# Optimization experiments

Hardware: AMD Instinct MI355X
Metric: run time of the kernel (lower is better)

Reference implementation:

```python
import jax, jax.numpy as jnp
import numpy as np

DIM = 512; HEADS = 8; DH = 64; M = 256; ITERS = 6; N_PATCH = 10000; N_CLASSES = 2


def layernorm(x, w, b, eps=1e-5):
    mu = x.mean(-1, keepdims=True)
    var = ((x - mu) ** 2).mean(-1, keepdims=True)
    return (x - mu) * jax.lax.rsqrt(var + eps) * w + b


def pinv_iter(x, iters=ITERS):
    # Moore-Penrose iterative pseudo-inverse (lucidrains nystrom-attention)
    abs_x = jnp.abs(x)
    col = abs_x.sum(-1)
    row = abs_x.sum(-2)
    z = jnp.swapaxes(x, -1, -2) / (jnp.max(col) * jnp.max(row))
    I = jnp.eye(x.shape[-1], dtype=x.dtype)
    for _ in range(iters):
        xz = x @ z
        z = 0.25 * z @ (13 * I - xz @ (15 * I - xz @ (7 * I - xz)))
    return z


def nystrom_attn(x, qkv_w, out_w, out_b, res_w):
    b, n, _ = x.shape
    pad = (-n) % M  # front-pad so n divisible by num_landmarks
    xp = jnp.pad(x, ((0, 0), (pad, 0), (0, 0)))
    npad = n + pad
    qkv = (xp @ qkv_w).reshape(b, npad, 3, HEADS, DH)
    q = jnp.transpose(qkv[:, :, 0], (0, 2, 1, 3)) * (DH ** -0.5)  # [b,h,n,d]
    k = jnp.transpose(qkv[:, :, 1], (0, 2, 1, 3))
    v = jnp.transpose(qkv[:, :, 2], (0, 2, 1, 3))
    l = npad // M
    q_l = q.reshape(b, HEADS, M, l, DH).mean(3)  # landmark means [b,h,m,d]
    k_l = k.reshape(b, HEADS, M, l, DH).mean(3)
    attn1 = jax.nn.softmax(jnp.einsum('bhnd,bhmd->bhnm', q, k_l), -1)
    attn2 = jax.nn.softmax(jnp.einsum('bhid,bhjd->bhij', q_l, k_l), -1)
    attn3 = jax.nn.softmax(jnp.einsum('bhmd,bhnd->bhmn', q_l, k), -1)
    out = (attn1 @ pinv_iter(attn2)) @ (attn3 @ v)  # [b,h,n,d]
    pk = (res_w.shape[2] - 1) // 2
    out = out + jax.lax.conv_general_dilated(
        v, res_w, (1, 1), [(pk, pk), (0, 0)], feature_group_count=HEADS)
    out = jnp.transpose(out, (0, 2, 1, 3)).reshape(b, npad, HEADS * DH)
    out = out @ out_w + out_b
    return out[:, -n:]


def ppeg(x, H, W, w7, b7, w5, b5, w3, b3):
    B, _, C = x.shape
    cls_tok, feat = x[:, :1], x[:, 1:]
    f = jnp.transpose(feat, (0, 2, 1)).reshape(B, C, H, W)
    def dw(w, b):
        p = w.shape[2] // 2
        return jax.lax.conv_general_dilated(
            f, w, (1, 1), [(p, p), (p, p)], feature_group_count=C) + b[None, :, None, None]
    y = f + dw(w7, b7) + dw(w5, b5) + dw(w3, b3)
    y = jnp.transpose(y.reshape(B, C, H * W), (0, 2, 1))
    return jnp.concatenate([cls_tok, y], axis=1)


def setup_inputs() -> dict:
    key = jax.random.key(0)
    ks = jax.random.split(key, 16)
    d = {
        'x': jax.random.normal(ks[0], (1, N_PATCH, DIM), jnp.float32),
        'cls_token': jax.random.normal(ks[1], (1, 1, DIM), jnp.float32) * 1e-6,
        'ln1_w': jnp.ones((DIM,), jnp.float32), 'ln1_b': jnp.zeros((DIM,), jnp.float32),
        'qkv1_w': jax.random.normal(ks[2], (DIM, 3 * DIM), jnp.float32) * 0.03,
        'out1_w': jax.random.normal(ks[3], (DIM, DIM), jnp.float32) * 0.04,
        'out1_b': jnp.zeros((DIM,), jnp.float32),
        'res1_w': jax.random.normal(ks[4], (HEADS, 1, 33, 1), jnp.float32) * 0.1,
        'p7_w': jax.random.normal(ks[5], (DIM, 1, 7, 7), jnp.float32) * 0.1,
        'p7_b': jnp.zeros((DIM,), jnp.float32),
        'p5_w': jax.random.normal(ks[6], (DIM, 1, 5, 5), jnp.float32) * 0.1,
        'p5_b': jnp.zeros((DIM,), jnp.float32),
        'p3_w': jax.random.normal(ks[7], (DIM, 1, 3, 3), jnp.float32) * 0.1,
        'p3_b': jnp.zeros((DIM,), jnp.float32),
        'ln2_w': jnp.ones((DIM,), jnp.float32), 'ln2_b': jnp.zeros((DIM,), jnp.float32),
        'qkv2_w': jax.random.normal(ks[8], (DIM, 3 * DIM), jnp.float32) * 0.03,
        'out2_w': jax.random.normal(ks[9], (DIM, DIM), jnp.float32) * 0.04,
        'out2_b': jnp.zeros((DIM,), jnp.float32),
        'res2_w': jax.random.normal(ks[10], (HEADS, 1, 33, 1), jnp.float32) * 0.1,
        'norm_w': jnp.ones((DIM,), jnp.float32), 'norm_b': jnp.zeros((DIM,), jnp.float32),
        'fc2_w': jax.random.normal(ks[11], (DIM, N_CLASSES), jnp.float32) * 0.06,
        'fc2_b': jnp.zeros((N_CLASSES,), jnp.float32),
        'pc_w': jax.random.normal(ks[12], (DIM, N_CLASSES), jnp.float32) * 0.06,
        'pc_b': jnp.zeros((N_CLASSES,), jnp.float32),
    }
    return d


def reference(x, cls_token, ln1_w, ln1_b, qkv1_w, out1_w, out1_b, res1_w,
              p7_w, p7_b, p5_w, p5_b, p3_w, p3_b,
              ln2_w, ln2_b, qkv2_w, out2_w, out2_b, res2_w,
              norm_w, norm_b, fc2_w, fc2_b, pc_w, pc_b):
    h = x.astype(jnp.float32)
    B, n0, C = h.shape
    _H = int(np.ceil(np.sqrt(n0))); _W = _H
    add = _H * _W - n0
    if add > 0:
        h = jnp.concatenate([h, h[:, :add]], axis=1)
    h = jnp.concatenate([jnp.broadcast_to(cls_token, (B, 1, C)), h], axis=1)
    h = h + nystrom_attn(layernorm(h, ln1_w, ln1_b), qkv1_w, out1_w, out1_b, res1_w)
    h = ppeg(h, _H, _W, p7_w, p7_b, p5_w, p5_b, p3_w, p3_b)
    h = h + nystrom_attn(layernorm(h, ln2_w, ln2_b), qkv2_w, out2_w, out2_b, res2_w)
    hn = layernorm(h, norm_w, norm_b)
    cls_f = hn[:, 0]
    patch_f = hn[:, 1:]
    if add > 0:
        patch_f = patch_f[:, :n0]
    bag_logits = cls_f @ fc2_w + fc2_b
    patch_logits = patch_f @ pc_w + pc_b
    patch_scores = jax.nn.softmax(patch_logits, -1)
    return bag_logits, patch_logits, patch_scores
```

## Files before the change

kernel.cpp:

```cpp
#include <hip/hip_runtime.h>
#include <hip/hip_bf16.h>

#define DIM    512
#define HEADS  8
#define DHD    64
#define MLAND  256
#define NTOK   10001
#define NPATCH 10000
#define NPAD   10240
#define PADR   239
#define LFAC   40
#define MOUT   10112
#define NSPLIT 8

typedef __bf16 bf16x8_t __attribute__((ext_vector_type(8)));
typedef float  f32x4_t  __attribute__((ext_vector_type(4)));
typedef short  short8_t __attribute__((ext_vector_type(8)));

__device__ inline bf16x8_t bzero8() {
    union { short8_t s; bf16x8_t b; } u;
    u.s = (short8_t){0, 0, 0, 0, 0, 0, 0, 0};
    return u.b;
}

#define GLDS(gp, lp) __builtin_amdgcn_global_load_lds( \
    (const __attribute__((address_space(1))) void*)(gp), \
    (__attribute__((address_space(3))) void*)(lp), 16, 0, 0)

__global__ void k_concat(const float* __restrict__ x, const float* __restrict__ cls,
                         float* __restrict__ h) {
    int idx = blockIdx.x * 256 + threadIdx.x;
    if (idx >= NTOK * DIM) return;
    int row = idx / DIM, col = idx % DIM;
    h[idx] = (row == 0) ? cls[col] : x[(row - 1) * DIM + col];
}

__global__ void k_layernorm_bf(const float* __restrict__ h, const float* __restrict__ w,
                               const float* __restrict__ b, __hip_bfloat16* __restrict__ xbf) {
    int row = blockIdx.x;
    const float* r = h + (long)row * DIM;
    int t = threadIdx.x;
    float v0 = r[t], v1 = r[t + 256];
    __shared__ float red[256];
    red[t] = v0 + v1; __syncthreads();
    for (int o = 128; o > 0; o >>= 1) { if (t < o) red[t] += red[t + o]; __syncthreads(); }
    float mu = red[0] * (1.f / DIM); __syncthreads();
    float d0 = v0 - mu, d1 = v1 - mu;
    red[t] = d0 * d0 + d1 * d1; __syncthreads();
    for (int o = 128; o > 0; o >>= 1) { if (t < o) red[t] += red[t + o]; __syncthreads(); }
    float rstd = rsqrtf(red[0] * (1.f / DIM) + 1e-5f);
    long base = (long)(PADR + row) * DIM;
    xbf[base + t]       = __float2bfloat16(d0 * rstd * w[t] + b[t]);
    xbf[base + t + 256] = __float2bfloat16(d1 * rstd * w[t + 256] + b[t + 256]);
}

__global__ void k_zerobf(__hip_bfloat16* __restrict__ p, int n) {
    int i = blockIdx.x * 256 + threadIdx.x;
    if (i < n) p[i] = __float2bfloat16(0.f);
}
__global__ void k_wt_cvt(const float* __restrict__ W, __hip_bfloat16* __restrict__ Wt,
                         int K, int N) {
    __shared__ float tile[32][33];
    int k0 = blockIdx.x * 32, n0 = blockIdx.y * 32;
    int lx = threadIdx.x % 32, ly = threadIdx.x / 32;
    for (int i = 0; i < 32; i += 8) tile[ly + i][lx] = W[(long)(k0 + ly + i) * N + n0 + lx];
    __syncthreads();
    for (int i = 0; i < 32; i += 8)
        Wt[(long)(n0 + ly + i) * K + k0 + lx] = __float2bfloat16(tile[lx][ly + i]);
}
__global__ void k_vt(const __hip_bfloat16* __restrict__ vh, __hip_bfloat16* __restrict__ vt) {
    __shared__ __hip_bfloat16 tile[32][33];
    int n0 = blockIdx.x * 32, d0 = blockIdx.y * 32, h = blockIdx.z;
    int lx = threadIdx.x % 32, ly = threadIdx.x / 32;
    for (int i = 0; i < 32; i += 8)
        tile[ly + i][lx] = vh[((long)h * NPAD + n0 + ly + i) * 64 + d0 + lx];
    __syncthreads();
    for (int i = 0; i < 32; i += 8)
        vt[((long)h * 64 + d0 + ly + i) * NPAD + n0 + lx] = tile[lx][ly + i];
}

__global__ __launch_bounds__(256) void k_qkv_gemm(
    const __hip_bfloat16* __restrict__ A, const __hip_bfloat16* __restrict__ Bt,
    __hip_bfloat16* __restrict__ qh, __hip_bfloat16* __restrict__ kh,
    __hip_bfloat16* __restrict__ vh)
{
    const int K = 512;
    __shared__ unsigned short As[128 * 64];
    __shared__ unsigned short Bs[128 * 64];
    int tid = threadIdx.x;
    int m0 = blockIdx.y * 128, n0 = blockIdx.x * 128;
    int wave = tid >> 6, lane = tid & 63;
    int wm = (wave & 1) * 64, wn = (wave >> 1) * 64;
    f32x4_t zero4 = {0.f, 0.f, 0.f, 0.f};
    f32x4_t acc[4][4];
#pragma unroll
    for (int i = 0; i < 4; i++)
#pragma unroll
        for (int j = 0; j < 4; j++) acc[i][j] = zero4;
    int quad = lane >> 4, fr = lane & 15;
    int lrow8 = lane >> 3, gls = lane & 7;
    int gg = gls ^ lrow8;

    for (int k0 = 0; k0 < K; k0 += 64) {
        __syncthreads();
#pragma unroll
        for (int rnd = 0; rnd < 4; rnd++) {
            int r0 = rnd * 32 + wave * 8;
            int ar = r0 + lrow8;
            GLDS(A  + (long)(m0 + ar) * K + k0 + gg * 8, &As[r0 * 64]);
            GLDS(Bt + (long)(n0 + ar) * K + k0 + gg * 8, &Bs[r0 * 64]);
        }
        __syncthreads();
#pragma unroll
        for (int ks = 0; ks < 2; ks++) {
            int sg = (ks * 4 + quad) ^ (fr & 7);
            bf16x8_t af[4], bq[4];
#pragma unroll
            for (int i = 0; i < 4; i++) {
                af[i] = *(const bf16x8_t*)&As[(wm + i * 16 + fr) * 64 + sg * 8];
                bq[i] = *(const bf16x8_t*)&Bs[(wn + i * 16 + fr) * 64 + sg * 8];
            }
#pragma unroll
            for (int i = 0; i < 4; i++)
#pragma unroll
                for (int j = 0; j < 4; j++)
                    acc[i][j] = __builtin_amdgcn_mfma_f32_16x16x32_bf16(af[i], bq[j], acc[i][j], 0, 0, 0);
        }
    }
    int col = lane & 15, rq = lane >> 4;
#pragma unroll
    for (int j = 0; j < 4; j++) {
        int c = n0 + wn + j * 16 + col;
        int sect = c >> 9;
        int hh = (c >> 6) & 7;
        int d = c & 63;
        __hip_bfloat16* dst = (sect == 0) ? qh : (sect == 1) ? kh : vh;
        float sc = (sect == 0) ? 0.125f : 1.f;
#pragma unroll
        for (int i = 0; i < 4; i++) {
            int rbase = m0 + wm + i * 16 + rq * 4;
#pragma unroll
            for (int rr = 0; rr < 4; rr++) {
                int r = rbase + rr;
                dst[((long)hh * NPAD + r) * 64 + d] = __float2bfloat16(acc[i][j][rr] * sc);
            }
        }
    }
}

__global__ __launch_bounds__(256) void k_mfma_gemm(
    const __hip_bfloat16* __restrict__ A, const __hip_bfloat16* __restrict__ Bt,
    float* __restrict__ C, int M, int N, int K, int Mstore,
    const float* __restrict__ bias, int accum)
{
    __shared__ unsigned short As[128 * 64];
    __shared__ unsigned short Bs[128 * 64];
    int tid = threadIdx.x;
    int m0 = blockIdx.y * 128, n0 = blockIdx.x * 128;
    int wave = tid >> 6, lane = tid & 63;
    int wm = (wave & 1) * 64, wn = (wave >> 1) * 64;
    f32x4_t zero4 = {0.f, 0.f, 0.f, 0.f};
    f32x4_t acc[4][4];
#pragma unroll
    for (int i = 0; i < 4; i++)
#pragma unroll
        for (int j = 0; j < 4; j++) acc[i][j] = zero4;
    int quad = lane >> 4, fr = lane & 15;
    int lrow8 = lane >> 3, gls = lane & 7;
    int gg = gls ^ lrow8;

    for (int k0 = 0; k0 < K; k0 += 64) {
        __syncthreads();
#pragma unroll
        for (int rnd = 0; rnd < 4; rnd++) {
            int r0 = rnd * 32 + wave * 8;
            int ar = r0 + lrow8;
            GLDS(A  + (long)(m0 + ar) * K + k0 + gg * 8, &As[r0 * 64]);
            GLDS(Bt + (long)(n0 + ar) * K + k0 + gg * 8, &Bs[r0 * 64]);
        }
        __syncthreads();
#pragma unroll
        for (int ks = 0; ks < 2; ks++) {
            int sg = (ks * 4 + quad) ^ (fr & 7);
            bf16x8_t af[4], bq[4];
#pragma unroll
            for (int i = 0; i < 4; i++) {
                af[i] = *(const bf16x8_t*)&As[(wm + i * 16 + fr) * 64 + sg * 8];
                bq[i] = *(const bf16x8_t*)&Bs[(wn + i * 16 + fr) * 64 + sg * 8];
            }
#pragma unroll
            for (int i = 0; i < 4; i++)
#pragma unroll
                for (int j = 0; j < 4; j++)
                    acc[i][j] = __builtin_amdgcn_mfma_f32_16x16x32_bf16(af[i], bq[j], acc[i][j], 0, 0, 0);
        }
    }
    int col = lane & 15, rq = lane >> 4;
#pragma unroll
    for (int j = 0; j < 4; j++) {
        int c = n0 + wn + j * 16 + col;
        float bsv = bias ? bias[c] : 0.f;
#pragma unroll
        for (int i = 0; i < 4; i++) {
            int rbase = m0 + wm + i * 16 + rq * 4;
#pragma unroll
            for (int rr = 0; rr < 4; rr++) {
                int r = rbase + rr;
                if (r >= Mstore) continue;
                float v = acc[i][j][rr] + bsv;
                long off = (long)r * N + c;
                if (accum) C[off] += v; else C[off] = v;
            }
        }
    }
}

__global__ __launch_bounds__(256) void k_mfma_t64(
    const __hip_bfloat16* __restrict__ A, long lda, long abatch, int arowmax,
    const __hip_bfloat16* __restrict__ Bt, long ldb, long bbatch,
    __hip_bfloat16* __restrict__ Cbf, long ldc, long cbatch, int ksplit)
{
    int h = blockIdx.z;
    const __hip_bfloat16* Ab = A + (long)h * abatch;
    const __hip_bfloat16* Bb = Bt + (long)h * bbatch;
    int m0 = blockIdx.y * 128;
    int kbeg = blockIdx.x * ksplit, kend = kbeg + ksplit;
    int wave = threadIdx.x >> 6, lane = threadIdx.x & 63;
    int wm = (wave & 1) * 64, wn = (wave >> 1) * 32;
    int fr = lane & 15, quad = lane >> 4;
    f32x4_t zero4 = {0.f, 0.f, 0.f, 0.f};
    f32x4_t acc[4][2];
#pragma unroll
    for (int i = 0; i < 4; i++) { acc[i][0] = zero4; acc[i][1] = zero4; }
    for (int k0 = kbeg; k0 < kend; k0 += 32) {
        bf16x8_t bq[2];
#pragma unroll
        for (int j = 0; j < 2; j++)
            bq[j] = *(const bf16x8_t*)(Bb + (long)(wn + j * 16 + fr) * ldb + k0 + quad * 8);
#pragma unroll
        for (int i = 0; i < 4; i++) {
            int r = m0 + wm + i * 16 + fr;
            bf16x8_t af = (r < arowmax) ? *(const bf16x8_t*)(Ab + (long)r * lda + k0 + quad * 8)
                                        : bzero8();
#pragma unroll
            for (int j = 0; j < 2; j++)
                acc[i][j] = __builtin_amdgcn_mfma_f32_16x16x32_bf16(af, bq[j], acc[i][j], 0, 0, 0);
        }
    }
#pragma unroll
    for (int i = 0; i < 4; i++)
#pragma unroll
        for (int j = 0; j < 2; j++)
#pragma unroll
            for (int rr = 0; rr < 4; rr++) {
                int r = m0 + wm + i * 16 + quad * 4 + rr;
                int c = wn + j * 16 + fr;
                Cbf[(long)h * cbatch + (long)c * ldc + r] = __float2bfloat16(acc[i][j][rr]);
            }
}

__global__ __launch_bounds__(256) void k_mm256(
    const __hip_bfloat16* __restrict__ Aa, const __hip_bfloat16* __restrict__ Bt,
    float s, float acoef, const __hip_bfloat16* __restrict__ Aadd,
    __hip_bfloat16* __restrict__ Ca, __hip_bfloat16* __restrict__ Ct)
{
    int hd = blockIdx.z;
    long hb = (long)hd * 65536;
    int m0 = blockIdx.y * 64, n0 = blockIdx.x * 32;
    int wave = threadIdx.x >> 6, lane = threadIdx.x & 63;
    int fr = lane & 15, quad = lane >> 4;
    int mrow = m0 + wave * 16;
    f32x4_t zero4 = {0.f, 0.f, 0.f, 0.f};
    f32x4_t acc[2];
    acc[0] = zero4; acc[1] = zero4;
#pragma unroll
    for (int k0 = 0; k0 < 256; k0 += 32) {
        bf16x8_t af = *(const bf16x8_t*)(Aa + hb + (long)(mrow + fr) * 256 + k0 + quad * 8);
#pragma unroll
        for (int j = 0; j < 2; j++) {
            bf16x8_t bq = *(const bf16x8_t*)(Bt + hb + (long)(n0 + j * 16 + fr) * 256 + k0 + quad * 8);
            acc[j] = __builtin_amdgcn_mfma_f32_16x16x32_bf16(af, bq, acc[j], 0, 0, 0);
        }
    }
#pragma unroll
    for (int j = 0; j < 2; j++)
#pragma unroll
        for (int rr = 0; rr < 4; rr++) {
            int r = mrow + quad * 4 + rr;
            int c = n0 + j * 16 + fr;
            float v = s * acc[j][rr];
            if (Aadd) v += acoef * __bfloat162float(Aadd[hb + (long)r * 256 + c]);
            __hip_bfloat16 bv = __float2bfloat16(v);
            if (Ca) Ca[hb + (long)r * 256 + c] = bv;
            if (Ct) Ct[hb + (long)c * 256 + r] = bv;
        }
}

__global__ __launch_bounds__(256) void k_attn3f(
    const __hip_bfloat16* __restrict__ qlbf, const __hip_bfloat16* __restrict__ kh,
    const __hip_bfloat16* __restrict__ vt, float* __restrict__ part)
{
    int ns = blockIdx.x, mt = blockIdx.y, h = blockIdx.z;
    int wave = threadIdx.x >> 6, lane = threadIdx.x & 63;
    int fr = lane & 15, quad = lane >> 4;
    int lrow8 = lane >> 3, gls = lane & 7;
    int gg = gls ^ lrow8;
    int vsub = lane >> 5, vgrp = lane & 31;
    int swz = fr & 7;
    __shared__ unsigned short Ks[2][256 * 64];
    __shared__ unsigned short Vs[2][64 * 256];
    __shared__ __hip_bfloat16 Pl[64 * 136];
    f32x4_t zero4 = {0.f, 0.f, 0.f, 0.f};
    bf16x8_t aq[2];
    {
        const __hip_bfloat16* qb = qlbf + (long)h * 16384 + (long)(mt * 64 + wave * 16 + fr) * 64;
        aq[0] = *(const bf16x8_t*)(qb + quad * 8);
        aq[1] = *(const bf16x8_t*)(qb + 32 + quad * 8);
    }
    f32x4_t O[4];
#pragma unroll
    for (int j = 0; j < 4; j++) O[j] = zero4;
    float mr[4] = {-1e30f, -1e30f, -1e30f, -1e30f};
    float lr[4] = {0.f, 0.f, 0.f, 0.f};
    const __hip_bfloat16* kb = kh + (long)h * NPAD * 64;
    const __hip_bfloat16* vb = vt + (long)h * 64 * NPAD;

#define STAGE_KV(N0, KD, VD) do { \
    _Pragma("unroll") \
    for (int rnd = 0; rnd < 8; rnd++) { \
        int r0 = rnd * 32 + wave * 8; \
        GLDS(kb + (long)((N0) + r0 + lrow8) * 64 + gg * 8, (KD) + r0 * 64); \
    } \
    _Pragma("unroll") \
    for (int rnd = 0; rnd < 8; rnd++) { \
        int v0 = rnd * 8 + wave * 2; \
        int vrow = v0 + vsub; \
        GLDS(vb + (long)vrow * NPAD + (N0) + (vgrp ^ (vrow & 7)) * 8, (VD) + v0 * 256); \
    } \
} while (0)

    STAGE_KV(ns * 1280, &Ks[0][0], &Vs[0][0]);

    for (int nt = 0; nt < 5; nt++) {
        int bsel = nt & 1;
        if (nt < 4) {
            int n1 = ns * 1280 + (nt + 1) * 256;
            STAGE_KV(n1, &Ks[bsel ^ 1][0], &Vs[bsel ^ 1][0]);
            asm volatile("s_waitcnt vmcnt(16)" ::: "memory");
        } else {
            asm volatile("s_waitcnt vmcnt(0)" ::: "memory");
        }
        __builtin_amdgcn_s_barrier();

        const unsigned short* Kc = &Ks[bsel][0];
        const unsigned short* Vc = &Vs[bsel][0];
        f32x4_t s[16];
#pragma unroll
        for (int j = 0; j < 16; j++) s[j] = zero4;
#pragma unroll
        for (int j = 0; j < 16; j++) {
            const unsigned short* kr = Kc + (j * 16 + fr) * 64;
            bf16x8_t b0 = *(const bf16x8_t*)(kr + (quad ^ swz) * 8);
            bf16x8_t b1 = *(const bf16x8_t*)(kr + ((quad ^ swz) ^ 4) * 8);
            s[j] = __builtin_amdgcn_mfma_f32_16x16x32_bf16(aq[0], b0, s[j], 0, 0, 0);
            s[j] = __builtin_amdgcn_mfma_f32_16x16x32_bf16(aq[1], b1, s[j], 0, 0, 0);
        }
        float tm[4] = {-1e30f, -1e30f, -1e30f, -1e30f};
#pragma unroll
        for (int j = 0; j < 16; j++)
#pragma unroll
            for (int rr = 0; rr < 4; rr++) tm[rr] = fmaxf(tm[rr], s[j][rr]);
#pragma unroll
        for (int rr = 0; rr < 4; rr++) {
#pragma unroll
            for (int o = 8; o > 0; o >>= 1) tm[rr] = fmaxf(tm[rr], __shfl_xor(tm[rr], o));
        }
        float alpha[4], ts[4];
#pragma unroll
        for (int rr = 0; rr < 4; rr++) {
            float mnew = fmaxf(mr[rr], tm[rr]);
            alpha[rr] = __expf(mr[rr] - mnew);
            mr[rr] = mnew;
            ts[rr] = 0.f;
        }
#pragma unroll
        for (int j = 0; j < 16; j++)
#pragma unroll
            for (int rr = 0; rr < 4; rr++) {
                float e = __expf(s[j][rr] - mr[rr]);
                s[j][rr] = e;
                ts[rr] += e;
            }
#pragma unroll
        for (int rr = 0; rr < 4; rr++) {
#pragma unroll
            for (int o = 8; o > 0; o >>= 1) ts[rr] += __shfl_xor(ts[rr], o);
            lr[rr] = lr[rr] * alpha[rr] + ts[rr];
        }
#pragma unroll
        for (int j = 0; j < 4; j++)
#pragma unroll
            for (int rr = 0; rr < 4; rr++) O[j][rr] *= alpha[rr];
#pragma unroll
        for (int half = 0; half < 2; half++) {
#pragma unroll
            for (int j = 0; j < 8; j++)
#pragma unroll
                for (int rr = 0; rr < 4; rr++)
                    Pl[(wave * 16 + quad * 4 + rr) * 136 + j * 16 + fr] =
                        __float2bfloat16(s[half * 8 + j][rr]);
#pragma unroll
            for (int k0 = 0; k0 < 128; k0 += 32) {
                bf16x8_t af = *(const bf16x8_t*)&Pl[(wave * 16 + fr) * 136 + k0 + quad * 8];
                int gb = (half * 128 + k0) >> 3;
#pragma unroll
                for (int j = 0; j < 4; j++) {
                    const unsigned short* vr = Vc + (j * 16 + fr) * 256;
                    bf16x8_t bq = *(const bf16x8_t*)(vr + ((gb + quad) ^ swz) * 8);
                    O[j] = __builtin_amdgcn_mfma_f32_16x16x32_bf16(af, bq, O[j], 0, 0, 0);
                }
            }
        }
        asm volatile("" ::: "memory");
        __builtin_amdgcn_s_barrier();
    }
#undef STAGE_KV

    float* Ob = part + (long)((h * 4 + mt) * NSPLIT + ns) * 4224;
#pragma unroll
    for (int j = 0; j < 4; j++)
#pragma unroll
        for (int rr = 0; rr < 4; rr++)
            Ob[(wave * 16 + quad * 4 + rr) * 64 + j * 16 + fr] = O[j][rr];
    if (fr == 0) {
#pragma unroll
        for (int rr = 0; rr < 4; rr++) {
            Ob[4096 + wave * 16 + quad * 4 + rr] = mr[rr];
            Ob[4160 + wave * 16 + quad * 4 + rr] = lr[rr];
        }
    }
}

__global__ void k_a3comb(const float* __restrict__ part, __hip_bfloat16* __restrict__ a3vt) {
    int mt = blockIdx.x, h = blockIdx.y, t = threadIdx.x;
    int row = t >> 2, c0 = (t & 3) * 16;
    long base = (long)((h * 4 + mt) * NSPLIT) * 4224;
    float M = -1e30f;
    for (int s = 0; s < NSPLIT; s++) M = fmaxf(M, part[base + s * 4224 + 4096 + row]);
    float L = 0.f;
    float o[16];
#pragma unroll
    for (int c = 0; c < 16; c++) o[c] = 0.f;
    for (int s = 0; s < NSPLIT; s++) {
        const float* pb = part + base + (long)s * 4224;
        float w = __expf(pb[4096 + row] - M);
        L += pb[4160 + row] * w;
#pragma unroll
        for (int c = 0; c < 16; c++) o[c] += w * pb[row * 64 + c0 + c];
    }
    float invL = 1.f / L;
#pragma unroll
    for (int c = 0; c < 16; c++)
        a3vt[(long)h * 16384 + (long)(c0 + c) * 256 + mt * 64 + row] = __float2bfloat16(o[c] * invL);
}

__global__ void k_conv_res(const __hip_bfloat16* __restrict__ vh, const float* __restrict__ resw,
                           __hip_bfloat16* __restrict__ convbf) {
    int e4 = blockIdx.x * 256 + threadIdx.x;
    if (e4 >= NTOK * 128) return;
    int i = e4 >> 7;
    int c4 = (e4 & 127) * 4;
    int hh = c4 >> 6, d = c4 & 63;
    int n = PADR + i;
    const __hip_bfloat16* vb = vh + (long)hh * NPAD * 64 + d;
    float a0 = 0.f, a1 = 0.f, a2 = 0.f, a3 = 0.f;
#pragma unroll
    for (int t = 0; t < 33; t++) {
        int nn = n - 16 + t;
        if (nn < NPAD) {
            float w = resw[hh * 33 + t];
            uint2 pv = *(const uint2*)(vb + (long)nn * 64);
            __hip_bfloat16 vv[4];
            *(uint2*)vv = pv;
            a0 += w * __bfloat162float(vv[0]);
            a1 += w * __bfloat162float(vv[1]);
            a2 += w * __bfloat162float(vv[2]);
            a3 += w * __bfloat162float(vv[3]);
        }
    }
    __hip_bfloat16 o[4] = {__float2bfloat16(a0), __float2bfloat16(a1),
                           __float2bfloat16(a2), __float2bfloat16(a3)};
    *(uint2*)(convbf + (long)i * DIM + c4) = *(uint2*)o;
}

__global__ __launch_bounds__(256) void k_attn1f(
    const __hip_bfloat16* __restrict__ qh, const __hip_bfloat16* __restrict__ klbf,
    const __hip_bfloat16* __restrict__ w2bt, const __hip_bfloat16* __restrict__ convbf,
    __hip_bfloat16* __restrict__ abf)
{
    int h = blockIdx.y;
    int i0 = blockIdx.x * 64;
    __shared__ __hip_bfloat16 Pl[64 * 136];
    int tid = threadIdx.x;
    int wave = tid >> 6, lane = tid & 63;
    int fr = lane & 15, quad = lane >> 4;
    const __hip_bfloat16* kb = klbf + (long)h * (MLAND * DHD);
    f32x4_t zero4 = {0.f, 0.f, 0.f, 0.f};
    float cpre[4][4];
#pragma unroll
    for (int j = 0; j < 4; j++)
#pragma unroll
        for (int rr = 0; rr < 4; rr++) {
            int r = i0 + wave * 16 + quad * 4 + rr;
            cpre[j][rr] = (r < NTOK)
                ? __bfloat162float(convbf[(long)r * DIM + h * DHD + j * 16 + fr]) : 0.f;
        }
    f32x4_t acc[16];
#pragma unroll
    for (int j = 0; j < 16; j++) acc[j] = zero4;
    int arow = i0 + wave * 16 + fr;
    const __hip_bfloat16* qrow = qh + ((long)h * NPAD + PADR + arow) * 64;
#pragma unroll
    for (int k0 = 0; k0 < 64; k0 += 32) {
        bf16x8_t af = (arow < NTOK) ? *(const bf16x8_t*)(qrow + k0 + quad * 8) : bzero8();
#pragma unroll
        for (int j = 0; j < 16; j++) {
            bf16x8_t bq = *(const bf16x8_t*)(kb + (long)(j * 16 + fr) * DHD + k0 + quad * 8);
            acc[j] = __builtin_amdgcn_mfma_f32_16x16x32_bf16(af, bq, acc[j], 0, 0, 0);
        }
    }
    float mx[4] = {-1e30f, -1e30f, -1e30f, -1e30f};
#pragma unroll
    for (int j = 0; j < 16; j++)
#pragma unroll
        for (int rr = 0; rr < 4; rr++) mx[rr] = fmaxf(mx[rr], acc[j][rr]);
#pragma unroll
    for (int rr = 0; rr < 4; rr++) {
#pragma unroll
        for (int o = 8; o > 0; o >>= 1) mx[rr] = fmaxf(mx[rr], __shfl_xor(mx[rr], o));
    }
    float sum[4] = {0.f, 0.f, 0.f, 0.f};
#pragma unroll
    for (int j = 0; j < 16; j++)
#pragma unroll
        for (int rr = 0; rr < 4; rr++) {
            float e = __expf(acc[j][rr] - mx[rr]);
            acc[j][rr] = e;
            sum[rr] += e;
        }
#pragma unroll
    for (int rr = 0; rr < 4; rr++) {
#pragma unroll
        for (int o = 8; o > 0; o >>= 1) sum[rr] += __shfl_xor(sum[rr], o);
    }
    const __hip_bfloat16* wb = w2bt + (long)h * (DHD * MLAND);
    f32x4_t oc[4];
#pragma unroll
    for (int j = 0; j < 4; j++) oc[j] = zero4;
#pragma unroll
    for (int half = 0; half < 2; half++) {
#pragma unroll
        for (int j = 0; j < 8; j++)
#pragma unroll
            for (int rr = 0; rr < 4; rr++)
                Pl[(wave * 16 + quad * 4 + rr) * 136 + j * 16 + fr] =
                    __float2bfloat16(acc[half * 8 + j][rr]);
#pragma unroll
        for (int k0 = 0; k0 < 128; k0 += 32) {
            bf16x8_t af = *(const bf16x8_t*)&Pl[(wave * 16 + fr) * 136 + k0 + quad * 8];
#pragma unroll
            for (int j = 0; j < 4; j++) {
                bf16x8_t bq = *(const bf16x8_t*)(wb + (long)(j * 16 + fr) * MLAND
                                                 + half * 128 + k0 + quad * 8);
                oc[j] = __builtin_amdgcn_mfma_f32_16x16x32_bf16(af, bq, oc[j], 0, 0, 0);
            }
        }
    }
    float invs[4];
#pragma unroll
    for (int rr = 0; rr < 4; rr++) invs[rr] = 1.f / sum[rr];
#pragma unroll
    for (int j = 0; j < 4; j++)
#pragma unroll
        for (int rr = 0; rr < 4; rr++) {
            int r = i0 + wave * 16 + quad * 4 + rr;
            if (r < NTOK) {
                long off = (long)r * DIM + h * DHD + j * 16 + fr;
                abf[off] = __float2bfloat16(cpre[j][rr] + oc[j][rr] * invs[rr]);
            }
        }
}

__global__ void k_landmarks(const __hip_bfloat16* __restrict__ qh,
                            const __hip_bfloat16* __restrict__ kh,
                            float* __restrict__ ql, float* __restrict__ kl,
                            __hip_bfloat16* __restrict__ qlbf, __hip_bfloat16* __restrict__ klbf) {
    int m = blockIdx.x, h = blockIdx.y, d = threadIdx.x;
    float sq = 0.f, sk = 0.f;
    for (int j = 0; j < LFAC; j++) {
        long base = ((long)h * NPAD + m * LFAC + j) * 64 + d;
        sq += __bfloat162float(qh[base]);
        sk += __bfloat162float(kh[base]);
    }
    long o = ((long)h * MLAND + m) * DHD + d;
    float vq = sq * (1.f / LFAC), vk = sk * (1.f / LFAC);
    ql[o] = vq; kl[o] = vk;
    qlbf[o] = __float2bfloat16(vq);
    klbf[o] = __float2bfloat16(vk);
}

__global__ void k_attn2(const float* __restrict__ ql, const float* __restrict__ kl,
                        float* __restrict__ attn2, __hip_bfloat16* __restrict__ attn2bf) {
    int i = blockIdx.x, h = blockIdx.y, j = threadIdx.x;
    __shared__ float q[64];
    __shared__ float red[256];
    if (j < 64) q[j] = ql[((long)h * MLAND + i) * DHD + j];
    __syncthreads();
    const float* kr = kl + ((long)h * MLAND + j) * DHD;
    float s = 0.f;
#pragma unroll 8
    for (int d = 0; d < 64; d++) s += q[d] * kr[d];
    red[j] = s; __syncthreads();
    for (int o = 128; o > 0; o >>= 1) { if (j < o) red[j] = fmaxf(red[j], red[j + o]); __syncthreads(); }
    float mx = red[0]; __syncthreads();
    float e = __expf(s - mx);
    red[j] = e; __syncthreads();
    for (int o = 128; o > 0; o >>= 1) { if (j < o) red[j] += red[j + o]; __syncthreads(); }
    float v = e / red[0];
    long off = ((long)h * MLAND + i) * MLAND + j;
    attn2[off] = v;
    attn2bf[off] = __float2bfloat16(v);
}

__global__ void k_colrow(const float* __restrict__ x, float* __restrict__ scal) {
    int h = blockIdx.x, t = threadIdx.x;
    const float* xh = x + (long)h * MLAND * MLAND;
    float cs = 0.f, rs = 0.f;
    for (int j = 0; j < MLAND; j++) {
        cs += fabsf(xh[(long)t * MLAND + j]);
        rs += fabsf(xh[(long)j * MLAND + t]);
    }
    __shared__ float red[256];
    red[t] = cs; __syncthreads();
    for (int o = 128; o > 0; o >>= 1) { if (t < o) red[t] = fmaxf(red[t], red[t + o]); __syncthreads(); }
    if (t == 0) scal[2 + h] = red[0];
    __syncthreads();
    red[t] = rs; __syncthreads();
    for (int o = 128; o > 0; o >>= 1) { if (t < o) red[t] = fmaxf(red[t], red[t + o]); __syncthreads(); }
    if (t == 0) scal[10 + h] = red[0];
}

__global__ void k_tscale2(const float* __restrict__ x, const float* __restrict__ scal,
                          __hip_bfloat16* __restrict__ za, __hip_bfloat16* __restrict__ zt) {
    int h = blockIdx.z;
    int tj = blockIdx.x * 32, ti = blockIdx.y * 32;
    __shared__ float tile[32][33];
    const float* xh = x + (long)h * 65536;
    int lx = threadIdx.x % 32, ly = threadIdx.x / 32;
    float cm = scal[2], rm = scal[10];
#pragma unroll
    for (int k = 1; k < 8; k++) {
        cm = fmaxf(cm, scal[2 + k]);
        rm = fmaxf(rm, scal[10 + k]);
    }
    float inv = 1.f / (cm * rm);
    for (int yy = 0; yy < 32; yy += 8) {
        float v = xh[(long)(ti + ly + yy) * MLAND + tj + lx];
        tile[ly + yy][lx] = v;
        zt[(long)h * 65536 + (long)(ti + ly + yy) * MLAND + tj + lx] = __float2bfloat16(v * inv);
    }
    __syncthreads();
    for (int yy = 0; yy < 32; yy += 8)
        za[(long)h * 65536 + (long)(tj + ly + yy) * MLAND + ti + lx] =
            __float2bfloat16(tile[lx][ly + yy] * inv);
}

__global__ void k_tfwd(const float* __restrict__ h, float* __restrict__ ft) {
    __shared__ float tile[32][33];
    int t0 = blockIdx.x * 32, c0 = blockIdx.y * 32;
    int lx = threadIdx.x % 32, ly = threadIdx.x / 32;
    for (int i = 0; i < 32; i += 8) {
        int t = t0 + ly + i;
        if (t < NPATCH) tile[ly + i][lx] = h[(long)(1 + t) * DIM + c0 + lx];
    }
    __syncthreads();
    for (int i = 0; i < 32; i += 8) {
        int c = c0 + ly + i, t = t0 + lx;
        if (t < NPATCH) ft[(long)c * NPATCH + t] = tile[lx][ly + i];
    }
}

__global__ __launch_bounds__(256) void k_ppeg2(
    const float* __restrict__ ft, float* __restrict__ yt,
    const float* __restrict__ w7, const float* __restrict__ b7,
    const float* __restrict__ w5, const float* __restrict__ b5,
    const float* __restrict__ w3, const float* __restrict__ b3)
{
    int s = blockIdx.x, c = blockIdx.y;
    __shared__ float tile[26][106];
    __shared__ float wt[49];
    int tid = threadIdx.x;
    int r0 = s * 20 - 3;
    for (int idx = tid; idx < 26 * 106; idx += 256) {
        int rr = idx / 106, cc = idx % 106;
        int gy = r0 + rr, gx = cc - 3;
        float v = 0.f;
        if (gy >= 0 && gy < 100 && gx >= 0 && gx < 100)
            v = ft[(long)c * NPATCH + gy * 100 + gx];
        tile[rr][cc] = v;
    }
    if (tid < 49) {
        int dy = tid / 7 - 3, dx = tid % 7 - 3;
        float w = w7[c * 49 + tid];
        if (dy >= -2 && dy <= 2 && dx >= -2 && dx <= 2) w += w5[c * 25 + (dy + 2) * 5 + (dx + 2)];
        if (dy >= -1 && dy <= 1 && dx >= -1 && dx <= 1) w += w3[c * 9 + (dy + 1) * 3 + (dx + 1)];
        wt[tid] = w;
    }
    __syncthreads();
    float bsum = b7[c] + b5[c] + b3[c];
    for (int p = tid; p < 2000; p += 256) {
        int ly = p / 100, lx = p % 100;
        float acc = tile[ly + 3][lx + 3] + bsum;
#pragma unroll
        for (int dy = 0; dy < 7; dy++)
#pragma unroll
            for (int dx = 0; dx < 7; dx++)
                acc += wt[dy * 7 + dx] * tile[ly + dy][lx + dx];
        yt[(long)c * NPATCH + (s * 20 + ly) * 100 + lx] = acc;
    }
}

__global__ void k_tback(const float* __restrict__ yt, float* __restrict__ h) {
    __shared__ float tile[32][33];
    int t0 = blockIdx.x * 32, c0 = blockIdx.y * 32;
    int lx = threadIdx.x % 32, ly = threadIdx.x / 32;
    for (int i = 0; i < 32; i += 8) {
        int c = c0 + ly + i, t = t0 + lx;
        if (t < NPATCH) tile[ly + i][lx] = yt[(long)c * NPATCH + t];
    }
    __syncthreads();
    for (int i = 0; i < 32; i += 8) {
        int t = t0 + ly + i;
        if (t < NPATCH) h[(long)(1 + t) * DIM + c0 + lx] = tile[lx][ly + i];
    }
}

__global__ void k_final(const float* __restrict__ h, const float* __restrict__ nw,
                        const float* __restrict__ nb,
                        const float* __restrict__ fc2w, const float* __restrict__ fc2b,
                        const float* __restrict__ pcw, const float* __restrict__ pcb,
                        float* __restrict__ out)
{
    int row = blockIdx.x;
    int t = threadIdx.x;
    const float* r = h + (long)row * DIM;
    float v0 = r[t], v1 = r[t + 256];
    __shared__ float red[256];
    red[t] = v0 + v1; __syncthreads();
    for (int o = 128; o > 0; o >>= 1) { if (t < o) red[t] += red[t + o]; __syncthreads(); }
    float mu = red[0] * (1.f / DIM); __syncthreads();
    float d0 = v0 - mu, d1 = v1 - mu;
    red[t] = d0 * d0 + d1 * d1; __syncthreads();
    for (int o = 128; o > 0; o >>= 1) { if (t < o) red[t] += red[t + o]; __syncthreads(); }
    float rstd = rsqrtf(red[0] * (1.f / DIM) + 1e-5f); __syncthreads();
    float h0 = d0 * rstd * nw[t] + nb[t];
    float h1 = d1 * rstd * nw[t + 256] + nb[t + 256];
    const float* w = (row == 0) ? fc2w : pcw;
    float p0 = h0 * w[t * 2] + h1 * w[(t + 256) * 2];
    float p1 = h0 * w[t * 2 + 1] + h1 * w[(t + 256) * 2 + 1];
    red[t] = p0; __syncthreads();
    for (int o = 128; o > 0; o >>= 1) { if (t < o) red[t] += red[t + o]; __syncthreads(); }
    float l0 = red[0]; __syncthreads();
    red[t] = p1; __syncthreads();
    for (int o = 128; o > 0; o >>= 1) { if (t < o) red[t] += red[t + o]; __syncthreads(); }
    if (t == 0) {
        float l1 = red[0];
        const float* bb = (row == 0) ? fc2b : pcb;
        float a0 = l0 + bb[0], a1 = l1 + bb[1];
        if (row == 0) { out[0] = a0; out[1] = a1; }
        else {
            long i = row - 1;
            out[2 + i * 2] = a0;
            out[2 + i * 2 + 1] = a1;
            float m = fmaxf(a0, a1);
            float e0 = __expf(a0 - m), e1 = __expf(a1 - m);
            float inv = 1.f / (e0 + e1);
            out[2 + 2 * NPATCH + i * 2] = e0 * inv;
            out[2 + 2 * NPATCH + i * 2 + 1] = e1 * inv;
        }
    }
}

extern "C" void kernel_launch(void* const* d_in, const int* in_sizes, int n_in,
                              void* d_out, int out_size, void* d_ws, size_t ws_size,
                              hipStream_t stream)
{
    const float* x     = (const float*)d_in[0];
    const float* cls   = (const float*)d_in[1];
    const float* ln1w  = (const float*)d_in[2];
    const float* ln1b  = (const float*)d_in[3];
    const float* qkv1w = (const float*)d_in[4];
    const float* out1w = (const float*)d_in[5];
    const float* out1b = (const float*)d_in[6];
    const float* res1w = (const float*)d_in[7];
    const float* p7w   = (const float*)d_in[8];
    const float* p7b   = (const float*)d_in[9];
    const float* p5w   = (const float*)d_in[10];
    const float* p5b   = (const float*)d_in[11];
    const float* p3w   = (const float*)d_in[12];
    const float* p3b   = (const float*)d_in[13];
    const float* ln2w  = (const float*)d_in[14];
    const float* ln2b  = (const float*)d_in[15];
    const float* qkv2w = (const float*)d_in[16];
    const float* out2w = (const float*)d_in[17];
    const float* out2b = (const float*)d_in[18];
    const float* res2w = (const float*)d_in[19];
    const float* normw = (const float*)d_in[20];
    const float* normb = (const float*)d_in[21];
    const float* fc2w  = (const float*)d_in[22];
    const float* fc2b  = (const float*)d_in[23];
    const float* pcw   = (const float*)d_in[24];
    const float* pcb   = (const float*)d_in[25];
    float* out = (float*)d_out;

    float* p = (float*)d_ws;
    float* h      = p; p += 5120512;
    float* yt     = p; p += 5120512;
    float* ql     = p; p += 131072;
    float* kl     = p; p += 131072;
    float* x2     = p; p += 524288;
    float* scal   = p; p += 32;
    float* part   = p; p += 1081344;
    float* ft     = p; p += 5120512;
    __hip_bfloat16* qh     = (__hip_bfloat16*)p; p += 2621440;
    __hip_bfloat16* kh     = (__hip_bfloat16*)p; p += 2621440;
    __hip_bfloat16* vh     = (__hip_bfloat16*)p; p += 2621440;
    __hip_bfloat16* xbf    = (__hip_bfloat16*)p; p += 2621440;
    __hip_bfloat16* abf    = (__hip_bfloat16*)p; p += 2588672;
    __hip_bfloat16* convbf = (__hip_bfloat16*)p; p += 2560256;
    __hip_bfloat16* qw1t   = (__hip_bfloat16*)p; p += 393216;
    __hip_bfloat16* qw2t   = (__hip_bfloat16*)p; p += 393216;
    __hip_bfloat16* ow1t   = (__hip_bfloat16*)p; p += 131072;
    __hip_bfloat16* ow2t   = (__hip_bfloat16*)p; p += 131072;
    __hip_bfloat16* x2a    = (__hip_bfloat16*)p; p += 262144;
    __hip_bfloat16* za     = (__hip_bfloat16*)p; p += 262144;
    __hip_bfloat16* zt     = (__hip_bfloat16*)p; p += 262144;
    __hip_bfloat16* za2    = (__hip_bfloat16*)p; p += 262144;
    __hip_bfloat16* zt2    = (__hip_bfloat16*)p; p += 262144;
    __hip_bfloat16* xza    = (__hip_bfloat16*)p; p += 262144;
    __hip_bfloat16* xzt    = (__hip_bfloat16*)p; p += 262144;
    __hip_bfloat16* t1t    = (__hip_bfloat16*)p; p += 262144;
    __hip_bfloat16* t2t    = (__hip_bfloat16*)p; p += 262144;
    __hip_bfloat16* qlbf   = (__hip_bfloat16*)p; p += 65536;
    __hip_bfloat16* klbf   = (__hip_bfloat16*)p; p += 65536;
    __hip_bfloat16* vt     = (__hip_bfloat16*)p; p += 2621440;
    __hip_bfloat16* a3vt   = (__hip_bfloat16*)p; p += 65536;
    __hip_bfloat16* w2bt   = (__hip_bfloat16*)p; p += 65536;

    k_concat<<<dim3((NTOK * DIM + 255) / 256), 256, 0, stream>>>(x, cls, h);
    k_wt_cvt<<<dim3(16, 48), 256, 0, stream>>>(qkv1w, qw1t, 512, 1536);
    k_wt_cvt<<<dim3(16, 48), 256, 0, stream>>>(qkv2w, qw2t, 512, 1536);
    k_wt_cvt<<<dim3(16, 16), 256, 0, stream>>>(out1w, ow1t, 512, 512);
    k_wt_cvt<<<dim3(16, 16), 256, 0, stream>>>(out2w, ow2t, 512, 512);
    k_zerobf<<<dim3((PADR * DIM + 255) / 256), 256, 0, stream>>>(xbf, PADR * DIM);

    auto layer = [&](const float* lnw, const float* lnb, const __hip_bfloat16* qwt,
                     const __hip_bfloat16* owt, const float* outb, const float* resw) {
        k_layernorm_bf<<<NTOK, 256, 0, stream>>>(h, lnw, lnb, xbf);
        k_qkv_gemm<<<dim3(12, 80), 256, 0, stream>>>(xbf, qwt, qh, kh, vh);
        k_vt<<<dim3(320, 2, HEADS), 256, 0, stream>>>(vh, vt);
        k_landmarks<<<dim3(MLAND, HEADS), 64, 0, stream>>>(qh, kh, ql, kl, qlbf, klbf);
        k_attn2<<<dim3(MLAND, HEADS), 256, 0, stream>>>(ql, kl, x2, x2a);
        k_colrow<<<HEADS, 256, 0, stream>>>(x2, scal);
        k_tscale2<<<dim3(8, 8, HEADS), 256, 0, stream>>>(x2, scal, za, zt);
        {
            __hip_bfloat16 *zra = za, *zrt = zt, *zoa = za2, *zot = zt2;
            dim3 g(8, 4, HEADS);
            for (int it = 0; it < 6; it++) {
                k_mm256<<<g, 256, 0, stream>>>(x2a, zrt, 1.f, 0.f, nullptr, xza, xzt);
                k_mm256<<<g, 256, 0, stream>>>(xza, xzt, -1.f, 7.f, xza, nullptr, t1t);
                k_mm256<<<g, 256, 0, stream>>>(xza, t1t, -1.f, 15.f, xza, nullptr, t2t);
                k_mm256<<<g, 256, 0, stream>>>(zra, t2t, -0.25f, 3.25f, zra, zoa, zot);
                __hip_bfloat16* tmp;
                tmp = zra; zra = zoa; zoa = tmp;
                tmp = zrt; zrt = zot; zot = tmp;
            }
        }
        k_attn3f<<<dim3(NSPLIT, 4, HEADS), 256, 0, stream>>>(qlbf, kh, vt, part);
        k_a3comb<<<dim3(4, HEADS), 256, 0, stream>>>(part, a3vt);
        k_mfma_t64<<<dim3(1, 2, HEADS), 256, 0, stream>>>(
            za, 256, 65536, 256, a3vt, 256, 16384,
            w2bt, 256, 16384, 256);
        k_conv_res<<<dim3((NTOK * 128 + 255) / 256), 256, 0, stream>>>(vh, resw, convbf);
        k_attn1f<<<dim3(157, HEADS), 256, 0, stream>>>(qh, klbf, w2bt, convbf, abf);
        k_mfma_gemm<<<dim3(4, 79), 256, 0, stream>>>(abf, owt, h, MOUT, 512, 512,
                                                     NTOK, outb, 1);
    };

    layer(ln1w, ln1b, qw1t, ow1t, out1b, res1w);

    k_tfwd<<<dim3(313, 16), 256, 0, stream>>>(h, ft);
    k_ppeg2<<<dim3(5, 512), 256, 0, stream>>>(ft, yt, p7w, p7b, p5w, p5b, p3w, p3b);
    k_tback<<<dim3(313, 16), 256, 0, stream>>>(yt, h);

    layer(ln2w, ln2b, qw2t, ow2t, out2b, res2w);

    k_final<<<NTOK, 256, 0, stream>>>(h, normw, normb, fc2w, fc2b, pcw, pcb, out);
    (void)in_sizes; (void)n_in; (void)out_size; (void)ws_size;
}
```

Baseline: 1.001 ms.

## Split attn1 landmark dimension across wave pairs with cross-wave softmax merge

Each block of the fused attn1 kernel now handles 32 rows instead of 64. The 256 landmarks are split into two halves, each processed by a separate wave pair that computes a partial softmax (max and sum). The partials are combined through shared memory with a rescaling factor, and the output contributions are summed through LDS before the residual conv term is added. The aim is to halve per-wave accumulator registers, double the grid size and raise occupancy (launch bounds 256,4), at the cost of extra barriers and an LDS exchange.

```diff
diff --git a/kernel.cpp b/kernel.cpp
--- a/kernel.cpp
+++ b/kernel.cpp
@@ -493,47 +493,41 @@
     *(uint2*)(convbf + (long)i * DIM + c4) = *(uint2*)o;
 }
 
-__global__ __launch_bounds__(256) void k_attn1f(
+__global__ __launch_bounds__(256, 4) void k_attn1f(
     const __hip_bfloat16* __restrict__ qh, const __hip_bfloat16* __restrict__ klbf,
     const __hip_bfloat16* __restrict__ w2bt, const __hip_bfloat16* __restrict__ convbf,
     __hip_bfloat16* __restrict__ abf)
 {
     int h = blockIdx.y;
-    int i0 = blockIdx.x * 64;
+    int i0 = blockIdx.x * 32;
     __shared__ __hip_bfloat16 Pl[64 * 136];
+    __shared__ float mS[2][2][16][2];
     int tid = threadIdx.x;
     int wave = tid >> 6, lane = tid & 63;
+    int rg = wave & 1, lh = wave >> 1;
     int fr = lane & 15, quad = lane >> 4;
-    const __hip_bfloat16* kb = klbf + (long)h * (MLAND * DHD);
+    const __hip_bfloat16* kb = klbf + (long)h * (MLAND * DHD) + (long)lh * 128 * DHD;
     f32x4_t zero4 = {0.f, 0.f, 0.f, 0.f};
-    float cpre[4][4];
-#pragma unroll
-    for (int j = 0; j < 4; j++)
-#pragma unroll
-        for (int rr = 0; rr < 4; rr++) {
-            int r = i0 + wave * 16 + quad * 4 + rr;
-            cpre[j][rr] = (r < NTOK)
-                ? __bfloat162float(convbf[(long)r * DIM + h * DHD + j * 16 + fr]) : 0.f;
-        }
-    f32x4_t acc[16];
-#pragma unroll
-    for (int j = 0; j < 16; j++) acc[j] = zero4;
-    int arow = i0 + wave * 16 + fr;
+
+    f32x4_t s[8];
+#pragma unroll
+    for (int j = 0; j < 8; j++) s[j] = zero4;
+    int arow = i0 + rg * 16 + fr;
     const __hip_bfloat16* qrow = qh + ((long)h * NPAD + PADR + arow) * 64;
 #pragma unroll
     for (int k0 = 0; k0 < 64; k0 += 32) {
         bf16x8_t af = (arow < NTOK) ? *(const bf16x8_t*)(qrow + k0 + quad * 8) : bzero8();
 #pragma unroll
-        for (int j = 0; j < 16; j++) {
+        for (int j = 0; j < 8; j++) {
             bf16x8_t bq = *(const bf16x8_t*)(kb + (long)(j * 16 + fr) * DHD + k0 + quad * 8);
-            acc[j] = __builtin_amdgcn_mfma_f32_16x16x32_bf16(af, bq, acc[j], 0, 0, 0);
+            s[j] = __builtin_amdgcn_mfma_f32_16x16x32_bf16(af, bq, s[j], 0, 0, 0);
         }
     }
     float mx[4] = {-1e30f, -1e30f, -1e30f, -1e30f};
 #pragma unroll
-    for (int j = 0; j < 16; j++)
-#pragma unroll
-        for (int rr = 0; rr < 4; rr++) mx[rr] = fmaxf(mx[rr], acc[j][rr]);
+    for (int j = 0; j < 8; j++)
+#pragma unroll
+        for (int rr = 0; rr < 4; rr++) mx[rr] = fmaxf(mx[rr], s[j][rr]);
 #pragma unroll
     for (int rr = 0; rr < 4; rr++) {
 #pragma unroll
@@ -541,11 +535,11 @@
     }
     float sum[4] = {0.f, 0.f, 0.f, 0.f};
 #pragma unroll
-    for (int j = 0; j < 16; j++)
+    for (int j = 0; j < 8; j++)
 #pragma unroll
         for (int rr = 0; rr < 4; rr++) {
-            float e = __expf(acc[j][rr] - mx[rr]);
-            acc[j][rr] = e;
+            float e = __expf(s[j][rr] - mx[rr]);
+            s[j][rr] = e;
             sum[rr] += e;
         }
 #pragma unroll
@@ -553,42 +547,78 @@
 #pragma unroll
         for (int o = 8; o > 0; o >>= 1) sum[rr] += __shfl_xor(sum[rr], o);
     }
-    const __hip_bfloat16* wb = w2bt + (long)h * (DHD * MLAND);
+    if (fr == 0) {
+#pragma unroll
+        for (int rr = 0; rr < 4; rr++) {
+            mS[lh][rg][quad * 4 + rr][0] = mx[rr];
+            mS[lh][rg][quad * 4 + rr][1] = sum[rr];
+        }
+    }
+#pragma unroll
+    for (int j = 0; j < 8; j++)
+#pragma unroll
+        for (int rr = 0; rr < 4; rr++)
+            Pl[(wave * 16 + quad * 4 + rr) * 136 + j * 16 + fr] = __float2bfloat16(s[j][rr]);
+    __syncthreads();
+    float fac[4];
+#pragma unroll
+    for (int rr = 0; rr < 4; rr++) {
+        int r16 = quad * 4 + rr;
+        float pm = mS[lh ^ 1][rg][r16][0], pS = mS[lh ^ 1][rg][r16][1];
+        float M = fmaxf(mx[rr], pm);
+        float sw = __expf(mx[rr] - M);
+        float tot = sum[rr] * sw + pS * __expf(pm - M);
+        fac[rr] = sw / tot;
+    }
+    const __hip_bfloat16* wb = w2bt + (long)h * (DHD * MLAND) + lh * 128;
     f32x4_t oc[4];
 #pragma unroll
     for (int j = 0; j < 4; j++) oc[j] = zero4;
 #pragma unroll
-    for (int half = 0; half < 2; half++) {
-#pragma unroll
-        for (int j = 0; j < 8; j++)
+    for (int k0 = 0; k0 < 128; k0 += 32) {
+        bf16x8_t af = *(const bf16x8_t*)&Pl[(wave * 16 + fr) * 136 + k0 + quad * 8];
+#pragma unroll
+        for (int j = 0; j < 4; j++) {
+            bf16x8_t bq = *(const bf16x8_t*)(wb + (long)(j * 16 + fr) * MLAND + k0 + quad * 8);
+            oc[j] = __builtin_amdgcn_mfma_f32_16x16x32_bf16(af, bq, oc[j], 0, 0, 0);
+        }
+    }
+#pragma unroll
+    for (int j = 0; j < 4; j++)
+#pragma unroll
+        for (int rr = 0; rr < 4; rr++) oc[j][rr] *= fac[rr];
+    __syncthreads();
+    float* ex = (float*)Pl;
+    if (lh == 1) {
+#pragma unroll
+        for (int j = 0; j < 4; j++)
 #pragma unroll
             for (int rr = 0; rr < 4; rr++)
-                Pl[(wave * 16 + quad * 4 + rr) * 136 + j * 16 + fr] =
-                    __float2bfloat16(acc[half * 8 + j][rr]);
-#pragma unroll
-        for (int k0 = 0; k0 < 128; k0 += 32) {
-            bf16x8_t af = *(const bf16x8_t*)&Pl[(wave * 16 + fr) * 136 + k0 + quad * 8];
-#pragma unroll
-            for (int j = 0; j < 4; j++) {
-                bf16x8_t bq = *(const bf16x8_t*)(wb + (long)(j * 16 + fr) * MLAND
-                                                 + half * 128 + k0 + quad * 8);
-                oc[j] = __builtin_amdgcn_mfma_f32_16x16x32_bf16(af, bq, oc[j], 0, 0, 0);
+                ex[(rg * 16 + quad * 4 + rr) * 64 + j * 16 + fr] = oc[j][rr];
+    }
+    __syncthreads();
+    if (lh == 0) {
+        float cp[4][4];
+#pragma unroll
+        for (int j = 0; j < 4; j++)
+#pragma unroll
+            for (int rr = 0; rr < 4; rr++) {
+                int r = i0 + rg * 16 + quad * 4 + rr;
+                cp[j][rr] = (r < NTOK)
+                    ? __bfloat162float(convbf[(long)r * DIM + h * DHD + j * 16 + fr]) : 0.f;
             }
-        }
-    }
-    float invs[4];
-#pragma unroll
-    for (int rr = 0; rr < 4; rr++) invs[rr] = 1.f / sum[rr];
-#pragma unroll
-    for (int j = 0; j < 4; j++)
-#pragma unroll
-        for (int rr = 0; rr < 4; rr++) {
-            int r = i0 + wave * 16 + quad * 4 + rr;
-            if (r < NTOK) {
-                long off = (long)r * DIM + h * DHD + j * 16 + fr;
-                abf[off] = __float2bfloat16(cpre[j][rr] + oc[j][rr] * invs[rr]);
+#pragma unroll
+        for (int j = 0; j < 4; j++)
+#pragma unroll
+            for (int rr = 0; rr < 4; rr++) {
+                int r = i0 + rg * 16 + quad * 4 + rr;
+                if (r < NTOK) {
+                    float v = oc[j][rr] + ex[(rg * 16 + quad * 4 + rr) * 64 + j * 16 + fr]
+                              + cp[j][rr];
+                    abf[(long)r * DIM + h * DHD + j * 16 + fr] = __float2bfloat16(v);
+                }
             }
-        }
+    }
 }
 
 __global__ void k_landmarks(const __hip_bfloat16* __restrict__ qh,
@@ -892,7 +922,7 @@
             za, 256, 65536, 256, a3vt, 256, 16384,
             w2bt, 256, 16384, 256);
         k_conv_res<<<dim3((NTOK * 128 + 255) / 256), 256, 0, stream>>>(vh, resw, convbf);
-        k_attn1f<<<dim3(157, HEADS), 256, 0, stream>>>(qh, klbf, w2bt, convbf, abf);
+        k_attn1f<<<dim3(313, HEADS), 256, 0, stream>>>(qh, klbf, w2bt, convbf, abf);
         k_mfma_gemm<<<dim3(4, 79), 256, 0, stream>>>(abf, owt, h, MOUT, 512, 512,
                                                      NTOK, outb, 1);
     };
```

Result: faster. 974.6 us (-2.6%).
